# Kernel tuning notes

Hardware: AMD Instinct MI355X
Metric: run time of the kernel (lower is better)

## Reference

```python
import jax, jax.numpy as jnp
import numpy as np

RADIUS = 0.4
NSAMPLE = 32


def setup_inputs() -> dict:
    key = jax.random.key(0)
    ks = jax.random.split(key, 6)
    B, N, C = 2, 16384, 64
    xyz = jax.random.normal(ks[0], (B, N, 3), jnp.float32)
    features = jax.random.normal(ks[1], (B, C, N), jnp.float32)

    def w(k, i, o):
        return jax.random.normal(k, (i, o), jnp.float32) * (1.0 / np.sqrt(i))

    W1 = w(ks[2], C + 3, 64)
    W2 = w(ks[3], 64, 64)
    W3 = w(ks[4], 64, 128)
    return {
        "xyz": xyz, "features": features,
        "W1": W1, "b1": jnp.zeros((64,), jnp.float32),
        "W2": W2, "b2": jnp.zeros((64,), jnp.float32),
        "W3": W3, "b3": jnp.zeros((128,), jnp.float32),
        "npoint": 4096,
    }


def ball_query(xyz, new_xyz, radius, nsample):
    """xyz [B,N,3], new_xyz [B,S,3] -> neighbor idx [B,S,nsample] int32.
    Replicates pointnet2 ball_query: first `nsample` points (in index order)
    within `radius` of each centroid; empty slots filled with the first hit
    (0 if no point is in range)."""
    N = xyz.shape[1]
    # squared distances [B,S,N] via ||a||^2 + ||b||^2 - 2 a.b
    d2 = (jnp.sum(new_xyz * new_xyz, -1)[:, :, None]
          + jnp.sum(xyz * xyz, -1)[:, None, :]
          - 2.0 * jnp.einsum('bsc,bnc->bsn', new_xyz, xyz))
    cand = jnp.where(d2 < radius * radius,
                     jnp.arange(N, dtype=jnp.int32), jnp.int32(N))
    neg_topk, _ = jax.lax.top_k(-cand, nsample)  # nsample smallest indices
    idx = -neg_topk
    first = idx[..., :1]
    idx = jnp.where(idx == N, first, idx)  # pad with first valid neighbor
    idx = jnp.where(idx == N, 0, idx)      # no neighbor at all -> 0
    return idx


def reference(xyz, features, W1, b1, W2, b2, W3, b3, npoint):
    B = xyz.shape[0]
    # sample_method=None, keep_first_half=False -> idx = arange(npoint)
    new_xyz = xyz[:, :npoint]                        # [B,S,3]
    idx = ball_query(jax.lax.stop_gradient(xyz),
                     jax.lax.stop_gradient(new_xyz), RADIUS, NSAMPLE)
    # group: gather neighbors, re-center xyz, concat features (use_xyz=True)
    grouped_xyz = jax.vmap(lambda p, i: p[i])(xyz, idx) - new_xyz[:, :, None]  # [B,S,K,3]
    feats_nc = features.transpose(0, 2, 1)           # [B,N,C]
    grouped_f = jax.vmap(lambda f, i: f[i])(feats_nc, idx)  # [B,S,K,C]
    g = jnp.concatenate([grouped_xyz, grouped_f], axis=-1)  # [B,S,K,3+C]
    # shared MLP (1x1 convs + ReLU)
    h = jax.nn.relu(jnp.einsum('bskc,cd->bskd', g, W1) + b1)
    h = jax.nn.relu(jnp.einsum('bskc,cd->bskd', h, W2) + b2)
    h = jax.nn.relu(jnp.einsum('bskc,cd->bskd', h, W3) + b3)
    new_features = jnp.max(h, axis=2).transpose(0, 2, 1)    # [B,128,S]
    samp_idx = jnp.tile(jnp.arange(npoint, dtype=jnp.int32), (B, 1))
    return new_xyz, new_features, samp_idx
```

## Files before the change

### kernel.cpp

```cpp
#include <hip/hip_runtime.h>

#define BB 2
#define NN 16384
#define CC 64
#define SS 4096
#define KK 32
#define R2 0.16f

typedef __bf16 bf16x8 __attribute__((ext_vector_type(8)));
typedef float  f32x4  __attribute__((ext_vector_type(4)));

#define MFMA(a, b, c) __builtin_amdgcn_mfma_f32_16x16x32_bf16((a), (b), (c), 0, 0, 0)

static __device__ __forceinline__ ushort f2bf(float f) {
    __bf16 h = (__bf16)f;
    return *(ushort*)&h;
}

#define WS_PTS4   0
#define WS_FEAT   524288
#define WS_W1T    4718592
#define WS_W2T    4730880
#define WS_W3T    4739072

#define T_PTS   (BB * NN)
#define T_W1    (T_PTS + 64 * 96)
#define T_W2    (T_W1 + 64 * 64)
#define T_W3    (T_W2 + 128 * 64)
#define T_NXYZ  (T_W3 + BB * SS * 3)
#define T_SIDX  (T_NXYZ + BB * SS)
#define T_ALL   (T_SIDX + BB * NN)

__global__ __launch_bounds__(256) void prep_kernel(
        const float* __restrict__ xyz, const float* __restrict__ feat,
        const float* __restrict__ W1, const float* __restrict__ W2,
        const float* __restrict__ W3,
        float4* __restrict__ pts4, ushort* __restrict__ feat_nc,
        ushort* __restrict__ W1t, ushort* __restrict__ W2t,
        ushort* __restrict__ W3t,
        float* __restrict__ out_xyz, float* __restrict__ out_sidx) {
    const int t = blockIdx.x * 256 + threadIdx.x;
    if (t < T_PTS) {
        const float* p = xyz + (size_t)t * 3;
        const float x = p[0], y = p[1], z = p[2];
        pts4[t] = make_float4(x, y, z, x * x + y * y + z * z);
    } else if (t < T_W1) {
        const int i = t - T_PTS;
        const int n = i / 96, k = i - n * 96;
        float v = 0.0f;
        if (k < 64) v = W1[(3 + k) * 64 + n];
        else if (k < 67) v = W1[(k - 64) * 64 + n];
        W1t[n * 96 + k] = f2bf(v);
    } else if (t < T_W2) {
        const int i = t - T_W1;
        const int n = i >> 6, k = i & 63;
        W2t[n * 64 + k] = f2bf(W2[k * 64 + n]);
    } else if (t < T_W3) {
        const int i = t - T_W2;
        const int n = i >> 6, k = i & 63;
        W3t[n * 64 + k] = f2bf(W3[k * 128 + n]);
    } else if (t < T_NXYZ) {
        const int i = t - T_W3;
        const int b = i / (SS * 3), j = i - b * (SS * 3);
        out_xyz[i] = xyz[(size_t)b * NN * 3 + j];
    } else if (t < T_SIDX) {
        const int i = t - T_NXYZ;
        out_sidx[i] = (float)(i & (SS - 1));
    } else if (t < T_ALL) {
        const int i = t - T_SIDX;
        const int b = i >> 14, n = i & (NN - 1);
        const float* fb = feat + (size_t)b * CC * NN + n;
        ushort* dst = feat_nc + (size_t)i * 64;
        #pragma unroll
        for (int c8 = 0; c8 < 8; ++c8) {
            uint u[4];
            #pragma unroll
            for (int j = 0; j < 4; ++j) {
                const float f0 = fb[(size_t)(c8 * 8 + 2 * j) * NN];
                const float f1 = fb[(size_t)(c8 * 8 + 2 * j + 1) * NN];
                u[j] = (uint)f2bf(f0) | ((uint)f2bf(f1) << 16);
            }
            *(uint4*)(dst + c8 * 8) = make_uint4(u[0], u[1], u[2], u[3]);
        }
    }
}

__global__ __launch_bounds__(256, 2) void fused_kernel(
        const float4* __restrict__ pts4, const ushort* __restrict__ feat_nc,
        const ushort* __restrict__ W1t, const ushort* __restrict__ W2t,
        const ushort* __restrict__ W3t,
        const float* __restrict__ b1, const float* __restrict__ b2,
        const float* __restrict__ b3, float* __restrict__ out_feat) {
    const int w = threadIdx.x >> 6, lane = threadIdx.x & 63;
    const int quad = lane >> 4, mrow = lane & 15;
    const int m = lane & 31, half = lane >> 5;

    __shared__ __align__(16) ushort ldsA[4][32 * 104];
    __shared__ float stage[128][5];
    ushort* gbuf = ldsA[w];
    int* hit = (int*)gbuf;

    const int xcd = blockIdx.x & 7;
    const int slot = blockIdx.x >> 3;
    const int b = xcd >> 2;
    const int s0 = ((xcd & 3) * 256 + slot) * 4;
    const int s = s0 + w;

    const float4* pb = pts4 + (size_t)b * NN;
    const ushort* fbase = feat_nc + (size_t)b * NN * 64;
    const unsigned long long ltmask = (1ull << lane) - 1ull;

    {
        const float4 c = pb[s];
        float4 p0 = pb[lane], p1 = pb[64 + lane];
        float4 p2 = pb[128 + lane], p3 = pb[192 + lane];
        int cnt = 0;
        for (int base = 0;;) {
            const int nb = base + 256;
            const bool last = nb >= NN;
            const int pf = last ? 0 : nb;
            const float4 q0 = pb[pf + lane], q1 = pb[pf + 64 + lane];
            const float4 q2 = pb[pf + 128 + lane], q3 = pb[pf + 192 + lane];

            const float d0 = c.w + p0.w - 2.0f * (c.x * p0.x + c.y * p0.y + c.z * p0.z);
            const float d1 = c.w + p1.w - 2.0f * (c.x * p1.x + c.y * p1.y + c.z * p1.z);
            const float d2 = c.w + p2.w - 2.0f * (c.x * p2.x + c.y * p2.y + c.z * p2.z);
            const float d3 = c.w + p3.w - 2.0f * (c.x * p3.x + c.y * p3.y + c.z * p3.z);
            const bool h0 = d0 < R2, h1 = d1 < R2, h2 = d2 < R2, h3 = d3 < R2;
            const unsigned long long m0 = __ballot(h0), m1 = __ballot(h1);
            const unsigned long long m2 = __ballot(h2), m3 = __ballot(h3);
            if ((m0 | m1 | m2 | m3) != 0ull) {
                const int c0 = __popcll(m0), c1 = __popcll(m1);
                const int c2 = __popcll(m2), c3 = __popcll(m3);
                if (h0) { const int p = cnt + __popcll(m0 & ltmask);                if (p < KK) hit[p] = base + lane; }
                if (h1) { const int p = cnt + c0 + __popcll(m1 & ltmask);           if (p < KK) hit[p] = base + 64 + lane; }
                if (h2) { const int p = cnt + c0 + c1 + __popcll(m2 & ltmask);      if (p < KK) hit[p] = base + 128 + lane; }
                if (h3) { const int p = cnt + c0 + c1 + c2 + __popcll(m3 & ltmask); if (p < KK) hit[p] = base + 192 + lane; }
                cnt += c0 + c1 + c2 + c3;
            }
            if (cnt >= KK || last) break;
            base = nb;
            p0 = q0; p1 = q1; p2 = q2; p3 = q3;
        }
        if (lane < KK) {
            const int v = (cnt == 0) ? 0 : ((lane < cnt) ? hit[lane] : hit[0]);
            hit[lane] = v;
        }
    }

    {
        const int sid = hit[m];
        const ushort* src = fbase + (size_t)sid * 64 + half * 32;
        ushort* dst = gbuf + m * 104 + half * 32;
        uint4 rows[4];
        #pragma unroll
        for (int i = 0; i < 4; ++i) rows[i] = *(const uint4*)(src + i * 8);
        const float4 p = pb[sid];
        const float4 cc = pb[s];
        #pragma unroll
        for (int i = 0; i < 4; ++i) *(uint4*)(dst + i * 8) = rows[i];
        if (half == 0) {
            bf16x8 rel = {(__bf16)(p.x - cc.x), (__bf16)(p.y - cc.y),
                          (__bf16)(p.z - cc.z), (__bf16)0.f,
                          (__bf16)0.f, (__bf16)0.f, (__bf16)0.f, (__bf16)0.f};
            *(bf16x8*)(gbuf + m * 104 + 64) = rel;
            *(uint4*)(gbuf + m * 104 + 88) = make_uint4(0, 0, 0, 0);
        } else {
            *(uint4*)(gbuf + m * 104 + 72) = make_uint4(0, 0, 0, 0);
            *(uint4*)(gbuf + m * 104 + 80) = make_uint4(0, 0, 0, 0);
        }
    }

    {
        f32x4 acc[2][4];
        #pragma unroll
        for (int nt = 0; nt < 4; ++nt) {
            const float bv = b1[nt * 16 + mrow];
            acc[0][nt] = (f32x4){bv, bv, bv, bv};
            acc[1][nt] = acc[0][nt];
        }
        #pragma unroll
        for (int ks = 0; ks < 3; ++ks) {
            const bf16x8 a0 = *(const bf16x8*)(gbuf + mrow * 104 + ks * 32 + quad * 8);
            const bf16x8 a1 = *(const bf16x8*)(gbuf + (16 + mrow) * 104 + ks * 32 + quad * 8);
            #pragma unroll
            for (int nt = 0; nt < 4; ++nt) {
                const bf16x8 wf = *(const bf16x8*)(W1t + (nt * 16 + mrow) * 96 + ks * 32 + quad * 8);
                acc[0][nt] = MFMA(a0, wf, acc[0][nt]);
                acc[1][nt] = MFMA(a1, wf, acc[1][nt]);
            }
        }
        #pragma unroll
        for (int mt = 0; mt < 2; ++mt)
            #pragma unroll
            for (int nt = 0; nt < 4; ++nt)
                #pragma unroll
                for (int r = 0; r < 4; ++r)
                    gbuf[(mt * 16 + quad * 4 + r) * 104 + nt * 16 + mrow] =
                        f2bf(fmaxf(acc[mt][nt][r], 0.0f));
    }

    {
        f32x4 acc[2][4];
        #pragma unroll
        for (int nt = 0; nt < 4; ++nt) {
            const float bv = b2[nt * 16 + mrow];
            acc[0][nt] = (f32x4){bv, bv, bv, bv};
            acc[1][nt] = acc[0][nt];
        }
        #pragma unroll
        for (int ks = 0; ks < 2; ++ks) {
            const bf16x8 a0 = *(const bf16x8*)(gbuf + mrow * 104 + ks * 32 + quad * 8);
            const bf16x8 a1 = *(const bf16x8*)(gbuf + (16 + mrow) * 104 + ks * 32 + quad * 8);
            #pragma unroll
            for (int nt = 0; nt < 4; ++nt) {
                const bf16x8 wf = *(const bf16x8*)(W2t + (nt * 16 + mrow) * 64 + ks * 32 + quad * 8);
                acc[0][nt] = MFMA(a0, wf, acc[0][nt]);
                acc[1][nt] = MFMA(a1, wf, acc[1][nt]);
            }
        }
        #pragma unroll
        for (int mt = 0; mt < 2; ++mt)
            #pragma unroll
            for (int nt = 0; nt < 4; ++nt)
                #pragma unroll
                for (int r = 0; r < 4; ++r)
                    gbuf[(mt * 16 + quad * 4 + r) * 104 + nt * 16 + mrow] =
                        f2bf(fmaxf(acc[mt][nt][r], 0.0f));
    }

    #pragma unroll
    for (int nh = 0; nh < 2; ++nh) {
        f32x4 acc[2][4];
        #pragma unroll
        for (int ntl = 0; ntl < 4; ++ntl) {
            const float bv = b3[(nh * 4 + ntl) * 16 + mrow];
            acc[0][ntl] = (f32x4){bv, bv, bv, bv};
            acc[1][ntl] = acc[0][ntl];
        }
        #pragma unroll
        for (int ks = 0; ks < 2; ++ks) {
            const bf16x8 a0 = *(const bf16x8*)(gbuf + mrow * 104 + ks * 32 + quad * 8);
            const bf16x8 a1 = *(const bf16x8*)(gbuf + (16 + mrow) * 104 + ks * 32 + quad * 8);
            #pragma unroll
            for (int ntl = 0; ntl < 4; ++ntl) {
                const bf16x8 wf = *(const bf16x8*)(
                    W3t + ((nh * 4 + ntl) * 16 + mrow) * 64 + ks * 32 + quad * 8);
                acc[0][ntl] = MFMA(a0, wf, acc[0][ntl]);
                acc[1][ntl] = MFMA(a1, wf, acc[1][ntl]);
            }
        }
        #pragma unroll
        for (int ntl = 0; ntl < 4; ++ntl) {
            const f32x4 v0 = acc[0][ntl], v1 = acc[1][ntl];
            float mx = fmaxf(fmaxf(v0[0], v0[1]), fmaxf(v0[2], v0[3]));
            mx = fmaxf(mx, fmaxf(fmaxf(v1[0], v1[1]), fmaxf(v1[2], v1[3])));
            mx = fmaxf(mx, __shfl_xor(mx, 16));
            mx = fmaxf(mx, __shfl_xor(mx, 32));
            mx = fmaxf(mx, 0.0f);
            if (quad == 0) stage[(nh * 4 + ntl) * 16 + mrow][w] = mx;
        }
    }
    __syncthreads();

    {
        const int ch = threadIdx.x & 127;
        const int hf = threadIdx.x >> 7;
        float* dst = out_feat + ((size_t)b * 128 + ch) * SS + s0 + hf * 2;
        *(float2*)dst = make_float2(stage[ch][hf * 2], stage[ch][hf * 2 + 1]);
    }
}

extern "C" void kernel_launch(void* const* d_in, const int* in_sizes, int n_in,
                              void* d_out, int out_size, void* d_ws, size_t ws_size,
                              hipStream_t stream) {
    const float* xyz  = (const float*)d_in[0];
    const float* feat = (const float*)d_in[1];
    const float* W1   = (const float*)d_in[2];
    const float* b1   = (const float*)d_in[3];
    const float* W2   = (const float*)d_in[4];
    const float* b2   = (const float*)d_in[5];
    const float* W3   = (const float*)d_in[6];
    const float* b3   = (const float*)d_in[7];

    float* out      = (float*)d_out;
    float* out_xyz  = out;
    float* out_feat = out + (size_t)BB * SS * 3;
    float* out_sidx = out_feat + (size_t)BB * 128 * SS;

    char* ws = (char*)d_ws;
    float4* pts4    = (float4*)(ws + WS_PTS4);
    ushort* feat_nc = (ushort*)(ws + WS_FEAT);
    ushort* W1t     = (ushort*)(ws + WS_W1T);
    ushort* W2t     = (ushort*)(ws + WS_W2T);
    ushort* W3t     = (ushort*)(ws + WS_W3T);

    prep_kernel<<<(T_ALL + 255) / 256, 256, 0, stream>>>(
        xyz, feat, W1, W2, W3, pts4, feat_nc, W1t, W2t, W3t, out_xyz, out_sidx);
    fused_kernel<<<BB * SS / 4, 256, 0, stream>>>(pts4, feat_nc, W1t, W2t, W3t,
                                                  b1, b2, b3, out_feat);
}
```

Measured before the change: 154.3 us.

## Replace brute-force ball query with uniform grid binning and neighbor-cell search

Builds a 32^3 uniform grid over the points using atomic counting, a prefix scan and a scatter into cell-sorted order. The ball query then scans only the 3x3 block of neighboring cell rows instead of a linear pass over all N points. Because candidates arrive out of index order, it collects up to CAP hits and selects the KK smallest indices with a binary search over ballots. It also splits the feature transpose across 8 threads per point. The cost is three extra launches, atomics and a memset, plus correctness risk if more than CAP hits overflow or points fall in clamped edge cells.

```diff
diff --git a/kernel.cpp b/kernel.cpp
--- a/kernel.cpp
+++ b/kernel.cpp
@@ -7,6 +7,11 @@
 #define KK 32
 #define R2 0.16f
 
+#define GD   32
+#define GC   (GD * GD * GD)
+#define CAP  1024
+#define CAPL (CAP / 64)
+
 typedef __bf16 bf16x8 __attribute__((ext_vector_type(8)));
 typedef float  f32x4  __attribute__((ext_vector_type(4)));
 
@@ -15,6 +20,11 @@
 static __device__ __forceinline__ ushort f2bf(float f) {
     __bf16 h = (__bf16)f;
     return *(ushort*)&h;
+}
+
+static __device__ __forceinline__ int cellc(float x) {
+    int i = (int)floorf(x * 2.5f + 16.0f);
+    return i < 0 ? 0 : (i > GD - 1 ? GD - 1 : i);
 }
 
 #define WS_PTS4   0
@@ -22,6 +32,10 @@
 #define WS_W1T    4718592
 #define WS_W2T    4730880
 #define WS_W3T    4739072
+#define WS_SPTS   4755456
+#define WS_SSID   5279744
+#define WS_CNT    5410816
+#define WS_OFF    5672960
 
 #define T_PTS   (BB * NN)
 #define T_W1    (T_PTS + 64 * 96)
@@ -29,7 +43,7 @@
 #define T_W3    (T_W2 + 128 * 64)
 #define T_NXYZ  (T_W3 + BB * SS * 3)
 #define T_SIDX  (T_NXYZ + BB * SS)
-#define T_ALL   (T_SIDX + BB * NN)
+#define T_ALL   (T_SIDX + BB * NN * 8)
 
 __global__ __launch_bounds__(256) void prep_kernel(
         const float* __restrict__ xyz, const float* __restrict__ feat,
@@ -38,12 +52,15 @@
         float4* __restrict__ pts4, ushort* __restrict__ feat_nc,
         ushort* __restrict__ W1t, ushort* __restrict__ W2t,
         ushort* __restrict__ W3t,
-        float* __restrict__ out_xyz, float* __restrict__ out_sidx) {
+        float* __restrict__ out_xyz, float* __restrict__ out_sidx,
+        uint* __restrict__ counts) {
     const int t = blockIdx.x * 256 + threadIdx.x;
     if (t < T_PTS) {
         const float* p = xyz + (size_t)t * 3;
         const float x = p[0], y = p[1], z = p[2];
         pts4[t] = make_float4(x, y, z, x * x + y * y + z * z);
+        const int cell = (((cellc(z) << 5) + cellc(y)) << 5) + cellc(x);
+        atomicAdd(&counts[(t >> 14) * GC + cell], 1u);
     } else if (t < T_W1) {
         const int i = t - T_PTS;
         const int n = i / 96, k = i - n * 96;
@@ -67,26 +84,69 @@
         const int i = t - T_NXYZ;
         out_sidx[i] = (float)(i & (SS - 1));
     } else if (t < T_ALL) {
-        const int i = t - T_SIDX;
-        const int b = i >> 14, n = i & (NN - 1);
+        const int j = t - T_SIDX;
+        const int nl = j >> 3, c8 = j & 7;
+        const int b = nl >> 14, n = nl & (NN - 1);
         const float* fb = feat + (size_t)b * CC * NN + n;
-        ushort* dst = feat_nc + (size_t)i * 64;
-        #pragma unroll
-        for (int c8 = 0; c8 < 8; ++c8) {
-            uint u[4];
-            #pragma unroll
-            for (int j = 0; j < 4; ++j) {
-                const float f0 = fb[(size_t)(c8 * 8 + 2 * j) * NN];
-                const float f1 = fb[(size_t)(c8 * 8 + 2 * j + 1) * NN];
-                u[j] = (uint)f2bf(f0) | ((uint)f2bf(f1) << 16);
-            }
-            *(uint4*)(dst + c8 * 8) = make_uint4(u[0], u[1], u[2], u[3]);
-        }
-    }
+        uint u[4];
+        #pragma unroll
+        for (int q = 0; q < 4; ++q) {
+            const float f0 = fb[(size_t)(c8 * 8 + 2 * q) * NN];
+            const float f1 = fb[(size_t)(c8 * 8 + 2 * q + 1) * NN];
+            u[q] = (uint)f2bf(f0) | ((uint)f2bf(f1) << 16);
+        }
+        *(uint4*)(feat_nc + (size_t)nl * 64 + c8 * 8) = make_uint4(u[0], u[1], u[2], u[3]);
+    }
+}
+
+__global__ __launch_bounds__(1024) void scan_kernel(uint* __restrict__ counts,
+                                                    uint* __restrict__ offs) {
+    __shared__ int lds[1024];
+    const int b = blockIdx.x, t = threadIdx.x;
+    uint* cnts = counts + (size_t)b * GC;
+    uint* off  = offs + (size_t)b * 32772;
+    int sum = 0;
+    #pragma unroll
+    for (int j = 0; j < 8; ++j) {
+        const uint4 v = *((const uint4*)cnts + t * 8 + j);
+        sum += (int)(v.x + v.y + v.z + v.w);
+    }
+    lds[t] = sum;
+    __syncthreads();
+    for (int d = 1; d < 1024; d <<= 1) {
+        const int add = (t >= d) ? lds[t - d] : 0;
+        __syncthreads();
+        lds[t] += add;
+        __syncthreads();
+    }
+    int run = lds[t] - sum;
+    #pragma unroll 4
+    for (int j = 0; j < 32; ++j) {
+        const int ci = t * 32 + j;
+        const uint cv = cnts[ci];
+        off[ci] = (uint)run;
+        cnts[ci] = (uint)run;
+        run += (int)cv;
+    }
+    if (t == 1023) off[GC] = (uint)run;
+}
+
+__global__ __launch_bounds__(256) void scatter_kernel(
+        const float4* __restrict__ pts4, uint* __restrict__ counts,
+        float4* __restrict__ spts, int* __restrict__ ssid) {
+    const int t = blockIdx.x * 256 + threadIdx.x;
+    const int b = t >> 14;
+    const float4 p = pts4[t];
+    const int cell = (((cellc(p.z) << 5) + cellc(p.y)) << 5) + cellc(p.x);
+    const uint pos = atomicAdd(&counts[(size_t)b * GC + cell], 1u);
+    spts[(size_t)b * NN + pos] = p;
+    ssid[(size_t)b * NN + pos] = t & (NN - 1);
 }
 
 __global__ __launch_bounds__(256, 2) void fused_kernel(
         const float4* __restrict__ pts4, const ushort* __restrict__ feat_nc,
+        const float4* __restrict__ spts, const int* __restrict__ ssid,
+        const uint* __restrict__ offs,
         const ushort* __restrict__ W1t, const ushort* __restrict__ W2t,
         const ushort* __restrict__ W3t,
         const float* __restrict__ b1, const float* __restrict__ b2,
@@ -112,39 +172,67 @@
 
     {
         const float4 c = pb[s];
-        float4 p0 = pb[lane], p1 = pb[64 + lane];
-        float4 p2 = pb[128 + lane], p3 = pb[192 + lane];
+        const int cx = cellc(c.x), cy = cellc(c.y), cz = cellc(c.z);
+        const int x0 = cx - 1 < 0 ? 0 : cx - 1;
+        const int x1 = cx + 1 > GD - 1 ? GD - 1 : cx + 1;
+        const uint* off = offs + (size_t)b * 32772;
+        const float4* sp = spts + (size_t)b * NN;
+        const int* sidp = ssid + (size_t)b * NN;
         int cnt = 0;
-        for (int base = 0;;) {
-            const int nb = base + 256;
-            const bool last = nb >= NN;
-            const int pf = last ? 0 : nb;
-            const float4 q0 = pb[pf + lane], q1 = pb[pf + 64 + lane];
-            const float4 q2 = pb[pf + 128 + lane], q3 = pb[pf + 192 + lane];
-
-            const float d0 = c.w + p0.w - 2.0f * (c.x * p0.x + c.y * p0.y + c.z * p0.z);
-            const float d1 = c.w + p1.w - 2.0f * (c.x * p1.x + c.y * p1.y + c.z * p1.z);
-            const float d2 = c.w + p2.w - 2.0f * (c.x * p2.x + c.y * p2.y + c.z * p2.z);
-            const float d3 = c.w + p3.w - 2.0f * (c.x * p3.x + c.y * p3.y + c.z * p3.z);
-            const bool h0 = d0 < R2, h1 = d1 < R2, h2 = d2 < R2, h3 = d3 < R2;
-            const unsigned long long m0 = __ballot(h0), m1 = __ballot(h1);
-            const unsigned long long m2 = __ballot(h2), m3 = __ballot(h3);
-            if ((m0 | m1 | m2 | m3) != 0ull) {
-                const int c0 = __popcll(m0), c1 = __popcll(m1);
-                const int c2 = __popcll(m2), c3 = __popcll(m3);
-                if (h0) { const int p = cnt + __popcll(m0 & ltmask);                if (p < KK) hit[p] = base + lane; }
-                if (h1) { const int p = cnt + c0 + __popcll(m1 & ltmask);           if (p < KK) hit[p] = base + 64 + lane; }
-                if (h2) { const int p = cnt + c0 + c1 + __popcll(m2 & ltmask);      if (p < KK) hit[p] = base + 128 + lane; }
-                if (h3) { const int p = cnt + c0 + c1 + c2 + __popcll(m3 & ltmask); if (p < KK) hit[p] = base + 192 + lane; }
-                cnt += c0 + c1 + c2 + c3;
-            }
-            if (cnt >= KK || last) break;
-            base = nb;
-            p0 = q0; p1 = q1; p2 = q2; p3 = q3;
-        }
-        if (lane < KK) {
-            const int v = (cnt == 0) ? 0 : ((lane < cnt) ? hit[lane] : hit[0]);
-            hit[lane] = v;
+        #pragma unroll
+        for (int e = 0; e < 9; ++e) {
+            const int z = cz + e / 3 - 1, y = cy + e % 3 - 1;
+            const bool ok = (z >= 0) && (z < GD) && (y >= 0) && (y < GD);
+            const int cb = ((z << 5) + y) << 5;
+            const int rs = ok ? (int)off[cb + x0] : 0;
+            const int re = ok ? (int)off[cb + x1 + 1] : 0;
+            for (int i0 = rs; i0 < re; i0 += 64) {
+                const int iw = i0 + lane;
+                const int ii = iw < re - 1 ? iw : re - 1;
+                const bool act = iw < re;
+                const float4 p = sp[ii];
+                const int id = sidp[ii];
+                const float d = c.w + p.w - 2.0f * (c.x * p.x + c.y * p.y + c.z * p.z);
+                const bool h = act && (d < R2);
+                const unsigned long long mk = __ballot(h);
+                if (mk != 0ull) {
+                    if (h) {
+                        const int pp = cnt + __popcll(mk & ltmask);
+                        if (pp < CAP) hit[pp] = id;
+                    }
+                    cnt += __popcll(mk);
+                }
+            }
+        }
+        if (cnt > KK) {
+            const int stored = cnt < CAP ? cnt : CAP;
+            int v[CAPL];
+            #pragma unroll
+            for (int j = 0; j < CAPL; ++j) {
+                const int q = j * 64 + lane;
+                v[j] = (q < stored) ? hit[q] : 0x7fffffff;
+            }
+            int lo = 0, hi = NN - 1;
+            while (lo < hi) {
+                const int mid = (lo + hi) >> 1;
+                int cle = 0;
+                #pragma unroll
+                for (int j = 0; j < CAPL; ++j) cle += (v[j] <= mid) ? 1 : 0;
+                #pragma unroll
+                for (int o = 1; o < 64; o <<= 1) cle += __shfl_xor(cle, o);
+                if (cle >= KK) hi = mid; else lo = mid + 1;
+            }
+            int pos = 0;
+            #pragma unroll
+            for (int j = 0; j < CAPL; ++j) {
+                const bool sel = v[j] <= lo;
+                const unsigned long long mk = __ballot(sel);
+                if (sel) hit[pos + __popcll(mk & ltmask)] = v[j];
+                pos += __popcll(mk);
+            }
+        } else if (lane < KK) {
+            const int vv = (cnt == 0) ? 0 : ((lane < cnt) ? hit[lane] : hit[0]);
+            hit[lane] = vv;
         }
     }
 
@@ -294,9 +382,18 @@
     ushort* W1t     = (ushort*)(ws + WS_W1T);
     ushort* W2t     = (ushort*)(ws + WS_W2T);
     ushort* W3t     = (ushort*)(ws + WS_W3T);
-
+    float4* spts    = (float4*)(ws + WS_SPTS);
+    int*    ssid    = (int*)(ws + WS_SSID);
+    uint*   counts  = (uint*)(ws + WS_CNT);
+    uint*   offs    = (uint*)(ws + WS_OFF);
+
+    hipMemsetAsync(counts, 0, (size_t)BB * GC * 4, stream);
     prep_kernel<<<(T_ALL + 255) / 256, 256, 0, stream>>>(
-        xyz, feat, W1, W2, W3, pts4, feat_nc, W1t, W2t, W3t, out_xyz, out_sidx);
-    fused_kernel<<<BB * SS / 4, 256, 0, stream>>>(pts4, feat_nc, W1t, W2t, W3t,
-                                                  b1, b2, b3, out_feat);
-}
+        xyz, feat, W1, W2, W3, pts4, feat_nc, W1t, W2t, W3t, out_xyz, out_sidx,
+        counts);
+    scan_kernel<<<BB, 1024, 0, stream>>>(counts, offs);
+    scatter_kernel<<<BB * NN / 256, 256, 0, stream>>>(pts4, counts, spts, ssid);
+    fused_kernel<<<BB * SS / 4, 256, 0, stream>>>(pts4, feat_nc, spts, ssid, offs,
+                                                  W1t, W2t, W3t, b1, b2, b3,
+                                                  out_feat);
+}
```

After: 168.3 us. +9.1%, slower.
